# Kernel tuning notes

Measured on AMD Instinct MI355X. Metric: run time of the kernel, lower is better.

The kernel has to match this reference:

```python
import jax, jax.numpy as jnp
import numpy as np

WIN = 8          # window_size
DIM = 96         # embedding dim
HEADS = 3        # num_heads
N = WIN * WIN    # tokens per window
B_ = 8192        # total windows (2 images * 64*64 windows)
NUM_WIN = 4096   # windows per image (mask leading dim)


def _relative_position_index():
    # Same construction as the torch module (meshgrid default 'ij').
    ch = np.arange(WIN)
    coords = np.stack(np.meshgrid(ch, ch, indexing="ij"))          # [2, W, W]
    flat = coords.reshape(2, -1)                                     # [2, N]
    rel = flat[:, :, None] - flat[:, None, :]                        # [2, N, N]
    rel = rel.transpose(1, 2, 0).astype(np.int32)                    # [N, N, 2]
    rel[:, :, 0] += WIN - 1
    rel[:, :, 1] += WIN - 1
    rel[:, :, 0] *= 2 * WIN - 1
    return rel.sum(-1)                                               # [N, N] int32


def setup_inputs() -> dict:
    key = jax.random.key(0)
    ks = jax.random.split(key, 8)
    x = jax.random.normal(ks[0], (B_, N, DIM), dtype=jnp.float32)
    mask = jax.random.normal(ks[1], (NUM_WIN, N, N), dtype=jnp.float32)
    s = 0.02
    qkv_w = jax.random.normal(ks[2], (3 * DIM, DIM), dtype=jnp.float32) * s
    qkv_b = jax.random.normal(ks[3], (3 * DIM,), dtype=jnp.float32) * s
    proj_w = jax.random.normal(ks[4], (DIM, DIM), dtype=jnp.float32) * s
    proj_b = jax.random.normal(ks[5], (DIM,), dtype=jnp.float32) * s
    n_bias = (2 * WIN - 1) * (2 * WIN - 1)  # 225
    bias_table = jax.random.normal(ks[6], (n_bias, HEADS), dtype=jnp.float32) * s
    rel_idx = jnp.asarray(_relative_position_index())  # [N, N] int32
    return {"x": x, "mask": mask, "qkv_w": qkv_w, "qkv_b": qkv_b,
            "proj_w": proj_w, "proj_b": proj_b, "bias_table": bias_table,
            "rel_idx": rel_idx}


def reference(x, mask, qkv_w, qkv_b, proj_w, proj_b, bias_table, rel_idx):
    Bw, n, C = x.shape
    hd = C // HEADS
    scale = hd ** (-0.5)
    qkv = (x @ qkv_w.T + qkv_b).reshape(Bw, n, 3, HEADS, hd)
    qkv = jnp.transpose(qkv, (2, 0, 3, 1, 4))
    q, k, v = qkv[0], qkv[1], qkv[2]
    attn = jnp.einsum("bhqd,bhkd->bhqk", q * scale, k)              # [Bw, H, n, n]
    # relative position bias gather: [n, n, H] -> [H, n, n]
    bias = bias_table[rel_idx.reshape(-1)].reshape(n, n, HEADS)
    attn = attn + jnp.transpose(bias, (2, 0, 1))[None]
    # shift mask: broadcast over (batch, heads)
    nw = mask.shape[0]
    attn = attn.reshape(Bw // nw, nw, HEADS, n, n) + mask[None, :, None]
    attn = attn.reshape(Bw, HEADS, n, n)
    attn = jax.nn.softmax(attn, axis=-1)
    out = jnp.einsum("bhqk,bhkd->bhqd", attn, v)                    # [Bw, H, n, hd]
    out = jnp.transpose(out, (0, 2, 1, 3)).reshape(Bw, n, C)
    return out @ proj_w.T + proj_b
```

## Files before the change

kernel.cpp:

```cpp
#include <hip/hip_runtime.h>

typedef __attribute__((ext_vector_type(8))) short short8v;
typedef __attribute__((ext_vector_type(4))) float f32x4;

#define INVLN2 1.4426950408889634f

__device__ __forceinline__ ushort f2bf(float f) {
  union { float f; unsigned int u; } c; c.f = f;
  return (ushort)((c.u + 0x7FFFu + ((c.u >> 16) & 1u)) >> 16);
}

__device__ __forceinline__ unsigned cvtpk(float a, float b) {
  unsigned r;
  asm("v_cvt_pk_bf16_f32 %0, %1, %2" : "=v"(r) : "v"(a), "v"(b));
  return r;
}

__device__ __forceinline__ float exp2w(float x) {
#if __has_builtin(__builtin_amdgcn_exp2f)
  return __builtin_amdgcn_exp2f(x);
#else
  return __expf(x * 0.6931471805599453f);
#endif
}

__device__ __forceinline__ short8v bits8(unsigned a, unsigned b, unsigned c, unsigned d) {
  union { unsigned u[4]; short8v s; } cv;
  cv.u[0] = a; cv.u[1] = b; cv.u[2] = c; cv.u[3] = d;
  return cv.s;
}

__global__ __launch_bounds__(256) void setup_k(
    const float* __restrict__ qkv_w, const float* __restrict__ proj_w,
    const float* __restrict__ bias_table, const int* __restrict__ rel_idx,
    const float* __restrict__ qkv_b,
    ushort* __restrict__ qkv_wb, ushort* __restrict__ proj_wb,
    float* __restrict__ bias_comb, float* __restrict__ qkv_bs) {
  const float qs = 0.17677669529663687f * INVLN2;
  int idx = blockIdx.x * 256 + threadIdx.x;
  if (idx < 27648) {
    qkv_wb[idx] = f2bf(qkv_w[idx] * (idx < 9216 ? qs : 1.0f));
  } else if (idx < 36864) {
    int i = idx - 27648;
    int cw = i / 96, j = i % 96;
    int h = j >> 5, kk = j & 31;
    int g = kk >> 3, b = (kk & 4) >> 2, d = kk & 3;
    int src = h * 32 + 16 * b + 4 * g + d;
    proj_wb[i] = f2bf(proj_w[cw * 96 + src]);
  } else if (idx < 49152) {
    int i = idx - 36864;
    int h = i / 4096, rc = i % 4096;
    bias_comb[i] = bias_table[rel_idx[rc] * 3 + h] * INVLN2;
  } else if (idx < 49440) {
    int i = idx - 49152;
    qkv_bs[i] = qkv_b[i] * (i < 96 ? qs : 1.0f);
  }
}

__global__ __launch_bounds__(256, 1) void winattn(
    const float* __restrict__ x, const float* __restrict__ mask,
    const ushort* __restrict__ qkv_wb, const ushort* __restrict__ proj_wb,
    const float* __restrict__ bias_comb, const float* __restrict__ qkv_bs,
    const float* __restrict__ proj_b, float* __restrict__ out) {
  __shared__ ushort klds[4][64][104];
  __shared__ ushort vts[4][96][64];
  __shared__ ushort wq[29952];

  const int bb = blockIdx.x;
  const int t = threadIdx.x;
  const int w = t >> 6;
  const int lane = t & 63;
  const int l15 = lane & 15;
  const int g = lane >> 4;
  const int qrow = w * 16 + l15;

  float4 xr4[4][3][2];
  #pragma unroll
  for (int u = 0; u < 4; ++u) {
    const int win = bb + ((u >> 1) << 11) + ((u & 1) << 12);
    const float* xr = x + ((size_t)win * 64 + qrow) * 96 + g * 8;
    #pragma unroll
    for (int ks3 = 0; ks3 < 3; ++ks3) {
      xr4[u][ks3][0] = *reinterpret_cast<const float4*>(xr + ks3 * 32);
      xr4[u][ks3][1] = *reinterpret_cast<const float4*>(xr + ks3 * 32 + 4);
    }
  }
  float4 mk4[2][4];
  #pragma unroll
  for (int p = 0; p < 2; ++p) {
    const float* mrow = mask + (size_t)(bb + (p << 11)) * 4096 + qrow * 64;
    #pragma unroll
    for (int tj = 0; tj < 4; ++tj)
      mk4[p][tj] = *reinterpret_cast<const float4*>(mrow + tj * 16 + g * 4);
  }

  #pragma unroll
  for (int i = 0; i < 14; ++i) {
    const int c = i * 256 + t;
    if (i < 13 || t < 128) {
      const int row = c / 12, cc = c % 12;
      short8v wv = *reinterpret_cast<const short8v*>(qkv_wb + row * 96 + cc * 8);
      *reinterpret_cast<short8v*>(&wq[row * 104 + cc * 8]) = wv;
    }
  }
  __syncthreads();

  short8v xa[4][3];
  #pragma unroll
  for (int u = 0; u < 4; ++u)
    #pragma unroll
    for (int ks3 = 0; ks3 < 3; ++ks3) {
      const float4 a0 = xr4[u][ks3][0], a1 = xr4[u][ks3][1];
      xa[u][ks3] = bits8(cvtpk(a0.x, a0.y), cvtpk(a0.z, a0.w),
                         cvtpk(a1.x, a1.y), cvtpk(a1.z, a1.w));
    }

  unsigned qpk[4][6][2];
  short8v bfA[3];
  float4 qbA = {0.f, 0.f, 0.f, 0.f}, qbB;
  float vbA = 0.f, vbB;
  {
    const ushort* wr = &wq[l15 * 104 + g * 8];
    bfA[0] = *reinterpret_cast<const short8v*>(wr);
    bfA[1] = *reinterpret_cast<const short8v*>(wr + 32);
    bfA[2] = *reinterpret_cast<const short8v*>(wr + 64);
    qbA = *reinterpret_cast<const float4*>(qkv_bs + g * 4);
  }
  #pragma unroll
  for (int nt = 0; nt < 18; ++nt) {
    short8v bfB[3];
    if (nt < 17) {
      const ushort* wr = &wq[((nt + 1) * 16 + l15) * 104 + g * 8];
      bfB[0] = *reinterpret_cast<const short8v*>(wr);
      bfB[1] = *reinterpret_cast<const short8v*>(wr + 32);
      bfB[2] = *reinterpret_cast<const short8v*>(wr + 64);
      if (nt + 1 < 12) qbB = *reinterpret_cast<const float4*>(qkv_bs + (nt + 1) * 16 + g * 4);
      else             vbB = qkv_bs[(nt + 1) * 16 + l15];
    }
    if (nt < 6) {
      #pragma unroll
      for (int u = 0; u < 4; ++u) {
        f32x4 acc = {0.f, 0.f, 0.f, 0.f};
        #pragma unroll
        for (int ks3 = 0; ks3 < 3; ++ks3)
          acc = __builtin_amdgcn_mfma_f32_16x16x32_bf16(bfA[ks3], xa[u][ks3], acc, 0, 0, 0);
        qpk[u][nt][0] = cvtpk(acc[0] + qbA.x, acc[1] + qbA.y);
        qpk[u][nt][1] = cvtpk(acc[2] + qbA.z, acc[3] + qbA.w);
      }
    } else if (nt < 12) {
      const int m = nt - 6;
      const int kcol = 32 * (m >> 1) + 8 * g + 4 * (m & 1);
      #pragma unroll
      for (int u = 0; u < 4; ++u) {
        f32x4 acc = {0.f, 0.f, 0.f, 0.f};
        #pragma unroll
        for (int ks3 = 0; ks3 < 3; ++ks3)
          acc = __builtin_amdgcn_mfma_f32_16x16x32_bf16(bfA[ks3], xa[u][ks3], acc, 0, 0, 0);
        uint2 pk = make_uint2(cvtpk(acc[0] + qbA.x, acc[1] + qbA.y),
                              cvtpk(acc[2] + qbA.z, acc[3] + qbA.w));
        *reinterpret_cast<uint2*>(&klds[u][qrow][kcol]) = pk;
      }
    } else {
      const int vc = nt * 16 + l15 - 192;
      const int tk = (32 * (w >> 1) + 8 * g + 4 * (w & 1)) ^ ((vc & 7) << 3);
      #pragma unroll
      for (int u = 0; u < 4; ++u) {
        f32x4 acc = {0.f, 0.f, 0.f, 0.f};
        #pragma unroll
        for (int ks3 = 0; ks3 < 3; ++ks3)
          acc = __builtin_amdgcn_mfma_f32_16x16x32_bf16(xa[u][ks3], bfA[ks3], acc, 0, 0, 0);
        uint2 pk = make_uint2(cvtpk(acc[0] + vbA, acc[1] + vbA),
                              cvtpk(acc[2] + vbA, acc[3] + vbA));
        *reinterpret_cast<uint2*>(&vts[u][vc][tk]) = pk;
      }
    }
    if (nt < 17) {
      bfA[0] = bfB[0]; bfA[1] = bfB[1]; bfA[2] = bfB[2];
      qbA = qbB; vbA = vbB;
    }
  }

  short8v qf[4][3];
  #pragma unroll
  for (int u = 0; u < 4; ++u)
    #pragma unroll
    for (int h = 0; h < 3; ++h)
      qf[u][h] = bits8(qpk[u][2 * h][0], qpk[u][2 * h][1],
                       qpk[u][2 * h + 1][0], qpk[u][2 * h + 1][1]);

  const float* bcb0 = bias_comb + qrow * 64;
  float bcf[3][4][4];
  #pragma unroll
  for (int h = 0; h < 3; ++h)
    #pragma unroll
    for (int tj = 0; tj < 4; ++tj) {
      float4 b4 = *reinterpret_cast<const float4*>(bcb0 + h * 4096 + tj * 16 + g * 4);
      bcf[h][tj][0] = b4.x; bcf[h][tj][1] = b4.y;
      bcf[h][tj][2] = b4.z; bcf[h][tj][3] = b4.w;
    }
  float mkp[2][4][4];
  #pragma unroll
  for (int p = 0; p < 2; ++p)
    #pragma unroll
    for (int tj = 0; tj < 4; ++tj) {
      mkp[p][tj][0] = mk4[p][tj].x * INVLN2;
      mkp[p][tj][1] = mk4[p][tj].y * INVLN2;
      mkp[p][tj][2] = mk4[p][tj].z * INVLN2;
      mkp[p][tj][3] = mk4[p][tj].w * INVLN2;
    }

  __syncthreads();

  short8v ofv[3][4];

  #pragma unroll
  for (int h = 0; h < 3; ++h) {
    f32x4 s[4][4];
    #pragma unroll
    for (int tj = 0; tj < 4; ++tj) {
      #pragma unroll
      for (int u = 0; u < 4; ++u) {
        short8v kf = *reinterpret_cast<const short8v*>(&klds[u][tj * 16 + l15][h * 32 + g * 8]);
        f32x4 z = {0.f, 0.f, 0.f, 0.f};
        s[u][tj] = __builtin_amdgcn_mfma_f32_16x16x32_bf16(kf, qf[u][h], z, 0, 0, 0);
      }
    }
    #pragma unroll
    for (int tj = 0; tj < 4; ++tj)
      #pragma unroll
      for (int r = 0; r < 4; ++r) {
        const float b0 = bcf[h][tj][r] + mkp[0][tj][r];
        const float b1 = bcf[h][tj][r] + mkp[1][tj][r];
        s[0][tj][r] += b0; s[1][tj][r] += b0;
        s[2][tj][r] += b1; s[3][tj][r] += b1;
      }
    float inv[4];
    #pragma unroll
    for (int u = 0; u < 4; ++u) {
      #pragma unroll
      for (int tj = 0; tj < 4; ++tj)
        #pragma unroll
        for (int r = 0; r < 4; ++r) s[u][tj][r] = exp2w(s[u][tj][r]);
      float sm = ((s[u][0][0] + s[u][0][1]) + (s[u][0][2] + s[u][0][3]))
               + ((s[u][1][0] + s[u][1][1]) + (s[u][1][2] + s[u][1][3]))
               + ((s[u][2][0] + s[u][2][1]) + (s[u][2][2] + s[u][2][3]))
               + ((s[u][3][0] + s[u][3][1]) + (s[u][3][2] + s[u][3][3]));
      sm += __shfl_xor(sm, 16);
      sm += __shfl_xor(sm, 32);
      inv[u] = __builtin_amdgcn_rcpf(sm);
    }
    short8v pfv[4][2];
    #pragma unroll
    for (int u = 0; u < 4; ++u) {
      unsigned p00 = cvtpk(s[u][0][0], s[u][0][1]);
      unsigned p01 = cvtpk(s[u][0][2], s[u][0][3]);
      unsigned p10 = cvtpk(s[u][1][0], s[u][1][1]);
      unsigned p11 = cvtpk(s[u][1][2], s[u][1][3]);
      unsigned p20 = cvtpk(s[u][2][0], s[u][2][1]);
      unsigned p21 = cvtpk(s[u][2][2], s[u][2][3]);
      unsigned p30 = cvtpk(s[u][3][0], s[u][3][1]);
      unsigned p31 = cvtpk(s[u][3][2], s[u][3][3]);
      pfv[u][0] = bits8(p00, p01, p10, p11);
      pfv[u][1] = bits8(p20, p21, p30, p31);
    }
    #pragma unroll
    for (int u = 0; u < 4; ++u) {
      f32x4 oacc[2];
      #pragma unroll
      for (int nt = 0; nt < 2; ++nt) {
        const int vc = h * 32 + nt * 16 + l15;
        f32x4 o = {0.f, 0.f, 0.f, 0.f};
        #pragma unroll
        for (int ks2 = 0; ks2 < 2; ++ks2) {
          const int tk = (ks2 * 32 + g * 8) ^ ((vc & 7) << 3);
          short8v vf = *reinterpret_cast<const short8v*>(&vts[u][vc][tk]);
          o = __builtin_amdgcn_mfma_f32_16x16x32_bf16(vf, pfv[u][ks2], o, 0, 0, 0);
        }
        oacc[nt] = o;
      }
      unsigned o00 = cvtpk(oacc[0][0] * inv[u], oacc[0][1] * inv[u]);
      unsigned o01 = cvtpk(oacc[0][2] * inv[u], oacc[0][3] * inv[u]);
      unsigned o10 = cvtpk(oacc[1][0] * inv[u], oacc[1][1] * inv[u]);
      unsigned o11 = cvtpk(oacc[1][2] * inv[u], oacc[1][3] * inv[u]);
      ofv[h][u] = bits8(o00, o01, o10, o11);
    }
  }

  f32x4 pacc[4][6];
  #pragma unroll
  for (int u = 0; u < 4; ++u)
    #pragma unroll
    for (int nt2 = 0; nt2 < 6; ++nt2) pacc[u][nt2] = (f32x4){0.f, 0.f, 0.f, 0.f};
  #pragma unroll
  for (int h = 0; h < 3; ++h) {
    #pragma unroll
    for (int nt2 = 0; nt2 < 6; ++nt2) {
      short8v pfw = *reinterpret_cast<const short8v*>(proj_wb + (nt2 * 16 + l15) * 96 + h * 32 + g * 8);
      #pragma unroll
      for (int u = 0; u < 4; ++u)
        pacc[u][nt2] = __builtin_amdgcn_mfma_f32_16x16x32_bf16(ofv[h][u], pfw, pacc[u][nt2], 0, 0, 0);
    }
  }

  float pb[6];
  #pragma unroll
  for (int nt2 = 0; nt2 < 6; ++nt2) pb[nt2] = proj_b[nt2 * 16 + l15];
  #pragma unroll
  for (int u = 0; u < 4; ++u) {
    const int win = bb + ((u >> 1) << 11) + ((u & 1) << 12);
    float* ob = out + (size_t)win * 6144 + (w * 16 + g * 4) * 96 + l15;
    #pragma unroll
    for (int nt2 = 0; nt2 < 6; ++nt2)
      #pragma unroll
      for (int r = 0; r < 4; ++r)
        ob[r * 96 + nt2 * 16] = pacc[u][nt2][r] + pb[nt2];
  }
}

extern "C" void kernel_launch(void* const* d_in, const int* in_sizes, int n_in,
                              void* d_out, int out_size, void* d_ws, size_t ws_size,
                              hipStream_t stream) {
  const float* x          = (const float*)d_in[0];
  const float* mask       = (const float*)d_in[1];
  const float* qkv_w      = (const float*)d_in[2];
  const float* qkv_b      = (const float*)d_in[3];
  const float* proj_w     = (const float*)d_in[4];
  const float* proj_b     = (const float*)d_in[5];
  const float* bias_table = (const float*)d_in[6];
  const int*   rel_idx    = (const int*)d_in[7];

  char* ws = (char*)d_ws;
  ushort* qkv_wb    = (ushort*)ws;
  ushort* proj_wb   = (ushort*)(ws + 55296);
  float*  bias_comb = (float*)(ws + 55296 + 18432);
  float*  qkv_bs    = (float*)(ws + 55296 + 18432 + 49152);

  setup_k<<<194, 256, 0, stream>>>(qkv_w, proj_w, bias_table, rel_idx, qkv_b,
                                   qkv_wb, proj_wb, bias_comb, qkv_bs);
  winattn<<<2048, 256, 0, stream>>>(x, mask, qkv_wb, proj_wb,
                                    bias_comb, qkv_bs, proj_b, (float*)d_out);
}
```

Baseline: 160.2 us.

## Make blocks process four window groups with register prefetch of next inputs

Each block now loops over four consecutive window groups instead of one, launching a quarter as many blocks. The bf16 QKV weights are staged into shared memory once per block and reused. The x and mask loads for the next group are issued right after the QKV stage so they overlap attention and projection compute. Extra barriers guard reuse of the K/V shared buffers, and holding the prefetched data in registers adds register pressure and coarser load balancing.

```diff
diff --git a/kernel.cpp b/kernel.cpp
--- a/kernel.cpp
+++ b/kernel.cpp
@@ -66,7 +66,6 @@
   __shared__ ushort vts[4][96][64];
   __shared__ ushort wq[29952];
 
-  const int bb = blockIdx.x;
   const int t = threadIdx.x;
   const int w = t >> 6;
   const int lane = t & 63;
@@ -75,23 +74,26 @@
   const int qrow = w * 16 + l15;
 
   float4 xr4[4][3][2];
-  #pragma unroll
-  for (int u = 0; u < 4; ++u) {
-    const int win = bb + ((u >> 1) << 11) + ((u & 1) << 12);
-    const float* xr = x + ((size_t)win * 64 + qrow) * 96 + g * 8;
-    #pragma unroll
-    for (int ks3 = 0; ks3 < 3; ++ks3) {
-      xr4[u][ks3][0] = *reinterpret_cast<const float4*>(xr + ks3 * 32);
-      xr4[u][ks3][1] = *reinterpret_cast<const float4*>(xr + ks3 * 32 + 4);
-    }
-  }
   float4 mk4[2][4];
-  #pragma unroll
-  for (int p = 0; p < 2; ++p) {
-    const float* mrow = mask + (size_t)(bb + (p << 11)) * 4096 + qrow * 64;
-    #pragma unroll
-    for (int tj = 0; tj < 4; ++tj)
-      mk4[p][tj] = *reinterpret_cast<const float4*>(mrow + tj * 16 + g * 4);
+  {
+    const int bb0 = blockIdx.x * 4;
+    #pragma unroll
+    for (int u = 0; u < 4; ++u) {
+      const int win = bb0 + ((u >> 1) << 11) + ((u & 1) << 12);
+      const float* xr = x + ((size_t)win * 64 + qrow) * 96 + g * 8;
+      #pragma unroll
+      for (int ks3 = 0; ks3 < 3; ++ks3) {
+        xr4[u][ks3][0] = *reinterpret_cast<const float4*>(xr + ks3 * 32);
+        xr4[u][ks3][1] = *reinterpret_cast<const float4*>(xr + ks3 * 32 + 4);
+      }
+    }
+    #pragma unroll
+    for (int p = 0; p < 2; ++p) {
+      const float* mrow = mask + (size_t)(bb0 + (p << 11)) * 4096 + qrow * 64;
+      #pragma unroll
+      for (int tj = 0; tj < 4; ++tj)
+        mk4[p][tj] = *reinterpret_cast<const float4*>(mrow + tj * 16 + g * 4);
+    }
   }
 
   #pragma unroll
@@ -105,89 +107,6 @@
   }
   __syncthreads();
 
-  short8v xa[4][3];
-  #pragma unroll
-  for (int u = 0; u < 4; ++u)
-    #pragma unroll
-    for (int ks3 = 0; ks3 < 3; ++ks3) {
-      const float4 a0 = xr4[u][ks3][0], a1 = xr4[u][ks3][1];
-      xa[u][ks3] = bits8(cvtpk(a0.x, a0.y), cvtpk(a0.z, a0.w),
-                         cvtpk(a1.x, a1.y), cvtpk(a1.z, a1.w));
-    }
-
-  unsigned qpk[4][6][2];
-  short8v bfA[3];
-  float4 qbA = {0.f, 0.f, 0.f, 0.f}, qbB;
-  float vbA = 0.f, vbB;
-  {
-    const ushort* wr = &wq[l15 * 104 + g * 8];
-    bfA[0] = *reinterpret_cast<const short8v*>(wr);
-    bfA[1] = *reinterpret_cast<const short8v*>(wr + 32);
-    bfA[2] = *reinterpret_cast<const short8v*>(wr + 64);
-    qbA = *reinterpret_cast<const float4*>(qkv_bs + g * 4);
-  }
-  #pragma unroll
-  for (int nt = 0; nt < 18; ++nt) {
-    short8v bfB[3];
-    if (nt < 17) {
-      const ushort* wr = &wq[((nt + 1) * 16 + l15) * 104 + g * 8];
-      bfB[0] = *reinterpret_cast<const short8v*>(wr);
-      bfB[1] = *reinterpret_cast<const short8v*>(wr + 32);
-      bfB[2] = *reinterpret_cast<const short8v*>(wr + 64);
-      if (nt + 1 < 12) qbB = *reinterpret_cast<const float4*>(qkv_bs + (nt + 1) * 16 + g * 4);
-      else             vbB = qkv_bs[(nt + 1) * 16 + l15];
-    }
-    if (nt < 6) {
-      #pragma unroll
-      for (int u = 0; u < 4; ++u) {
-        f32x4 acc = {0.f, 0.f, 0.f, 0.f};
-        #pragma unroll
-        for (int ks3 = 0; ks3 < 3; ++ks3)
-          acc = __builtin_amdgcn_mfma_f32_16x16x32_bf16(bfA[ks3], xa[u][ks3], acc, 0, 0, 0);
-        qpk[u][nt][0] = cvtpk(acc[0] + qbA.x, acc[1] + qbA.y);
-        qpk[u][nt][1] = cvtpk(acc[2] + qbA.z, acc[3] + qbA.w);
-      }
-    } else if (nt < 12) {
-      const int m = nt - 6;
-      const int kcol = 32 * (m >> 1) + 8 * g + 4 * (m & 1);
-      #pragma unroll
-      for (int u = 0; u < 4; ++u) {
-        f32x4 acc = {0.f, 0.f, 0.f, 0.f};
-        #pragma unroll
-        for (int ks3 = 0; ks3 < 3; ++ks3)
-          acc = __builtin_amdgcn_mfma_f32_16x16x32_bf16(bfA[ks3], xa[u][ks3], acc, 0, 0, 0);
-        uint2 pk = make_uint2(cvtpk(acc[0] + qbA.x, acc[1] + qbA.y),
-                              cvtpk(acc[2] + qbA.z, acc[3] + qbA.w));
-        *reinterpret_cast<uint2*>(&klds[u][qrow][kcol]) = pk;
-      }
-    } else {
-      const int vc = nt * 16 + l15 - 192;
-      const int tk = (32 * (w >> 1) + 8 * g + 4 * (w & 1)) ^ ((vc & 7) << 3);
-      #pragma unroll
-      for (int u = 0; u < 4; ++u) {
-        f32x4 acc = {0.f, 0.f, 0.f, 0.f};
-        #pragma unroll
-        for (int ks3 = 0; ks3 < 3; ++ks3)
-          acc = __builtin_amdgcn_mfma_f32_16x16x32_bf16(xa[u][ks3], bfA[ks3], acc, 0, 0, 0);
-        uint2 pk = make_uint2(cvtpk(acc[0] + vbA, acc[1] + vbA),
-                              cvtpk(acc[2] + vbA, acc[3] + vbA));
-        *reinterpret_cast<uint2*>(&vts[u][vc][tk]) = pk;
-      }
-    }
-    if (nt < 17) {
-      bfA[0] = bfB[0]; bfA[1] = bfB[1]; bfA[2] = bfB[2];
-      qbA = qbB; vbA = vbB;
-    }
-  }
-
-  short8v qf[4][3];
-  #pragma unroll
-  for (int u = 0; u < 4; ++u)
-    #pragma unroll
-    for (int h = 0; h < 3; ++h)
-      qf[u][h] = bits8(qpk[u][2 * h][0], qpk[u][2 * h][1],
-                       qpk[u][2 * h + 1][0], qpk[u][2 * h + 1][1]);
-
   const float* bcb0 = bias_comb + qrow * 64;
   float bcf[3][4][4];
   #pragma unroll
@@ -198,122 +117,232 @@
       bcf[h][tj][0] = b4.x; bcf[h][tj][1] = b4.y;
       bcf[h][tj][2] = b4.z; bcf[h][tj][3] = b4.w;
     }
-  float mkp[2][4][4];
-  #pragma unroll
-  for (int p = 0; p < 2; ++p)
-    #pragma unroll
-    for (int tj = 0; tj < 4; ++tj) {
-      mkp[p][tj][0] = mk4[p][tj].x * INVLN2;
-      mkp[p][tj][1] = mk4[p][tj].y * INVLN2;
-      mkp[p][tj][2] = mk4[p][tj].z * INVLN2;
-      mkp[p][tj][3] = mk4[p][tj].w * INVLN2;
-    }
-
-  __syncthreads();
-
-  short8v ofv[3][4];
-
-  #pragma unroll
-  for (int h = 0; h < 3; ++h) {
-    f32x4 s[4][4];
-    #pragma unroll
-    for (int tj = 0; tj < 4; ++tj) {
-      #pragma unroll
-      for (int u = 0; u < 4; ++u) {
-        short8v kf = *reinterpret_cast<const short8v*>(&klds[u][tj * 16 + l15][h * 32 + g * 8]);
-        f32x4 z = {0.f, 0.f, 0.f, 0.f};
-        s[u][tj] = __builtin_amdgcn_mfma_f32_16x16x32_bf16(kf, qf[u][h], z, 0, 0, 0);
-      }
-    }
-    #pragma unroll
-    for (int tj = 0; tj < 4; ++tj)
-      #pragma unroll
-      for (int r = 0; r < 4; ++r) {
-        const float b0 = bcf[h][tj][r] + mkp[0][tj][r];
-        const float b1 = bcf[h][tj][r] + mkp[1][tj][r];
-        s[0][tj][r] += b0; s[1][tj][r] += b0;
-        s[2][tj][r] += b1; s[3][tj][r] += b1;
-      }
-    float inv[4];
-    #pragma unroll
-    for (int u = 0; u < 4; ++u) {
-      #pragma unroll
-      for (int tj = 0; tj < 4; ++tj)
-        #pragma unroll
-        for (int r = 0; r < 4; ++r) s[u][tj][r] = exp2w(s[u][tj][r]);
-      float sm = ((s[u][0][0] + s[u][0][1]) + (s[u][0][2] + s[u][0][3]))
-               + ((s[u][1][0] + s[u][1][1]) + (s[u][1][2] + s[u][1][3]))
-               + ((s[u][2][0] + s[u][2][1]) + (s[u][2][2] + s[u][2][3]))
-               + ((s[u][3][0] + s[u][3][1]) + (s[u][3][2] + s[u][3][3]));
-      sm += __shfl_xor(sm, 16);
-      sm += __shfl_xor(sm, 32);
-      inv[u] = __builtin_amdgcn_rcpf(sm);
-    }
-    short8v pfv[4][2];
-    #pragma unroll
-    for (int u = 0; u < 4; ++u) {
-      unsigned p00 = cvtpk(s[u][0][0], s[u][0][1]);
-      unsigned p01 = cvtpk(s[u][0][2], s[u][0][3]);
-      unsigned p10 = cvtpk(s[u][1][0], s[u][1][1]);
-      unsigned p11 = cvtpk(s[u][1][2], s[u][1][3]);
-      unsigned p20 = cvtpk(s[u][2][0], s[u][2][1]);
-      unsigned p21 = cvtpk(s[u][2][2], s[u][2][3]);
-      unsigned p30 = cvtpk(s[u][3][0], s[u][3][1]);
-      unsigned p31 = cvtpk(s[u][3][2], s[u][3][3]);
-      pfv[u][0] = bits8(p00, p01, p10, p11);
-      pfv[u][1] = bits8(p20, p21, p30, p31);
-    }
-    #pragma unroll
-    for (int u = 0; u < 4; ++u) {
-      f32x4 oacc[2];
-      #pragma unroll
-      for (int nt = 0; nt < 2; ++nt) {
-        const int vc = h * 32 + nt * 16 + l15;
-        f32x4 o = {0.f, 0.f, 0.f, 0.f};
-        #pragma unroll
-        for (int ks2 = 0; ks2 < 2; ++ks2) {
-          const int tk = (ks2 * 32 + g * 8) ^ ((vc & 7) << 3);
-          short8v vf = *reinterpret_cast<const short8v*>(&vts[u][vc][tk]);
-          o = __builtin_amdgcn_mfma_f32_16x16x32_bf16(vf, pfv[u][ks2], o, 0, 0, 0);
-        }
-        oacc[nt] = o;
-      }
-      unsigned o00 = cvtpk(oacc[0][0] * inv[u], oacc[0][1] * inv[u]);
-      unsigned o01 = cvtpk(oacc[0][2] * inv[u], oacc[0][3] * inv[u]);
-      unsigned o10 = cvtpk(oacc[1][0] * inv[u], oacc[1][1] * inv[u]);
-      unsigned o11 = cvtpk(oacc[1][2] * inv[u], oacc[1][3] * inv[u]);
-      ofv[h][u] = bits8(o00, o01, o10, o11);
-    }
-  }
-
-  f32x4 pacc[4][6];
-  #pragma unroll
-  for (int u = 0; u < 4; ++u)
-    #pragma unroll
-    for (int nt2 = 0; nt2 < 6; ++nt2) pacc[u][nt2] = (f32x4){0.f, 0.f, 0.f, 0.f};
-  #pragma unroll
-  for (int h = 0; h < 3; ++h) {
-    #pragma unroll
-    for (int nt2 = 0; nt2 < 6; ++nt2) {
-      short8v pfw = *reinterpret_cast<const short8v*>(proj_wb + (nt2 * 16 + l15) * 96 + h * 32 + g * 8);
-      #pragma unroll
-      for (int u = 0; u < 4; ++u)
-        pacc[u][nt2] = __builtin_amdgcn_mfma_f32_16x16x32_bf16(ofv[h][u], pfw, pacc[u][nt2], 0, 0, 0);
-    }
-  }
-
   float pb[6];
   #pragma unroll
   for (int nt2 = 0; nt2 < 6; ++nt2) pb[nt2] = proj_b[nt2 * 16 + l15];
-  #pragma unroll
-  for (int u = 0; u < 4; ++u) {
-    const int win = bb + ((u >> 1) << 11) + ((u & 1) << 12);
-    float* ob = out + (size_t)win * 6144 + (w * 16 + g * 4) * 96 + l15;
-    #pragma unroll
-    for (int nt2 = 0; nt2 < 6; ++nt2)
-      #pragma unroll
-      for (int r = 0; r < 4; ++r)
-        ob[r * 96 + nt2 * 16] = pacc[u][nt2][r] + pb[nt2];
+
+  for (int j = 0; j < 4; ++j) {
+    const int bb = blockIdx.x * 4 + j;
+
+    short8v xa[4][3];
+    #pragma unroll
+    for (int u = 0; u < 4; ++u)
+      #pragma unroll
+      for (int ks3 = 0; ks3 < 3; ++ks3) {
+        const float4 a0 = xr4[u][ks3][0], a1 = xr4[u][ks3][1];
+        xa[u][ks3] = bits8(cvtpk(a0.x, a0.y), cvtpk(a0.z, a0.w),
+                           cvtpk(a1.x, a1.y), cvtpk(a1.z, a1.w));
+      }
+    float mkp[2][4][4];
+    #pragma unroll
+    for (int p = 0; p < 2; ++p)
+      #pragma unroll
+      for (int tj = 0; tj < 4; ++tj) {
+        mkp[p][tj][0] = mk4[p][tj].x * INVLN2;
+        mkp[p][tj][1] = mk4[p][tj].y * INVLN2;
+        mkp[p][tj][2] = mk4[p][tj].z * INVLN2;
+        mkp[p][tj][3] = mk4[p][tj].w * INVLN2;
+      }
+
+    unsigned qpk[4][6][2];
+    short8v bfA[3];
+    float4 qbA = {0.f, 0.f, 0.f, 0.f}, qbB;
+    float vbA = 0.f, vbB;
+    {
+      const ushort* wr = &wq[l15 * 104 + g * 8];
+      bfA[0] = *reinterpret_cast<const short8v*>(wr);
+      bfA[1] = *reinterpret_cast<const short8v*>(wr + 32);
+      bfA[2] = *reinterpret_cast<const short8v*>(wr + 64);
+      qbA = *reinterpret_cast<const float4*>(qkv_bs + g * 4);
+    }
+    #pragma unroll
+    for (int nt = 0; nt < 18; ++nt) {
+      short8v bfB[3];
+      if (nt < 17) {
+        const ushort* wr = &wq[((nt + 1) * 16 + l15) * 104 + g * 8];
+        bfB[0] = *reinterpret_cast<const short8v*>(wr);
+        bfB[1] = *reinterpret_cast<const short8v*>(wr + 32);
+        bfB[2] = *reinterpret_cast<const short8v*>(wr + 64);
+        if (nt + 1 < 12) qbB = *reinterpret_cast<const float4*>(qkv_bs + (nt + 1) * 16 + g * 4);
+        else             vbB = qkv_bs[(nt + 1) * 16 + l15];
+      }
+      if (nt < 6) {
+        #pragma unroll
+        for (int u = 0; u < 4; ++u) {
+          f32x4 acc = {0.f, 0.f, 0.f, 0.f};
+          #pragma unroll
+          for (int ks3 = 0; ks3 < 3; ++ks3)
+            acc = __builtin_amdgcn_mfma_f32_16x16x32_bf16(bfA[ks3], xa[u][ks3], acc, 0, 0, 0);
+          qpk[u][nt][0] = cvtpk(acc[0] + qbA.x, acc[1] + qbA.y);
+          qpk[u][nt][1] = cvtpk(acc[2] + qbA.z, acc[3] + qbA.w);
+        }
+      } else if (nt < 12) {
+        const int m = nt - 6;
+        const int kcol = 32 * (m >> 1) + 8 * g + 4 * (m & 1);
+        #pragma unroll
+        for (int u = 0; u < 4; ++u) {
+          f32x4 acc = {0.f, 0.f, 0.f, 0.f};
+          #pragma unroll
+          for (int ks3 = 0; ks3 < 3; ++ks3)
+            acc = __builtin_amdgcn_mfma_f32_16x16x32_bf16(bfA[ks3], xa[u][ks3], acc, 0, 0, 0);
+          uint2 pk = make_uint2(cvtpk(acc[0] + qbA.x, acc[1] + qbA.y),
+                                cvtpk(acc[2] + qbA.z, acc[3] + qbA.w));
+          *reinterpret_cast<uint2*>(&klds[u][qrow][kcol]) = pk;
+        }
+      } else {
+        const int vc = nt * 16 + l15 - 192;
+        const int tk = (32 * (w >> 1) + 8 * g + 4 * (w & 1)) ^ ((vc & 7) << 3);
+        #pragma unroll
+        for (int u = 0; u < 4; ++u) {
+          f32x4 acc = {0.f, 0.f, 0.f, 0.f};
+          #pragma unroll
+          for (int ks3 = 0; ks3 < 3; ++ks3)
+            acc = __builtin_amdgcn_mfma_f32_16x16x32_bf16(xa[u][ks3], bfA[ks3], acc, 0, 0, 0);
+          uint2 pk = make_uint2(cvtpk(acc[0] + vbA, acc[1] + vbA),
+                                cvtpk(acc[2] + vbA, acc[3] + vbA));
+          *reinterpret_cast<uint2*>(&vts[u][vc][tk]) = pk;
+        }
+      }
+      if (nt < 17) {
+        bfA[0] = bfB[0]; bfA[1] = bfB[1]; bfA[2] = bfB[2];
+        qbA = qbB; vbA = vbB;
+      }
+    }
+
+    short8v qf[4][3];
+    #pragma unroll
+    for (int u = 0; u < 4; ++u)
+      #pragma unroll
+      for (int h = 0; h < 3; ++h)
+        qf[u][h] = bits8(qpk[u][2 * h][0], qpk[u][2 * h][1],
+                         qpk[u][2 * h + 1][0], qpk[u][2 * h + 1][1]);
+
+    __syncthreads();
+
+    if (j < 3) {
+      const int bbn = bb + 1;
+      #pragma unroll
+      for (int u = 0; u < 4; ++u) {
+        const int win = bbn + ((u >> 1) << 11) + ((u & 1) << 12);
+        const float* xr = x + ((size_t)win * 64 + qrow) * 96 + g * 8;
+        #pragma unroll
+        for (int ks3 = 0; ks3 < 3; ++ks3) {
+          xr4[u][ks3][0] = *reinterpret_cast<const float4*>(xr + ks3 * 32);
+          xr4[u][ks3][1] = *reinterpret_cast<const float4*>(xr + ks3 * 32 + 4);
+        }
+      }
+      #pragma unroll
+      for (int p = 0; p < 2; ++p) {
+        const float* mrow = mask + (size_t)(bbn + (p << 11)) * 4096 + qrow * 64;
+        #pragma unroll
+        for (int tj = 0; tj < 4; ++tj)
+          mk4[p][tj] = *reinterpret_cast<const float4*>(mrow + tj * 16 + g * 4);
+      }
+    }
+
+    short8v ofv[3][4];
+
+    #pragma unroll
+    for (int h = 0; h < 3; ++h) {
+      f32x4 s[4][4];
+      #pragma unroll
+      for (int tj = 0; tj < 4; ++tj) {
+        #pragma unroll
+        for (int u = 0; u < 4; ++u) {
+          short8v kf = *reinterpret_cast<const short8v*>(&klds[u][tj * 16 + l15][h * 32 + g * 8]);
+          f32x4 z = {0.f, 0.f, 0.f, 0.f};
+          s[u][tj] = __builtin_amdgcn_mfma_f32_16x16x32_bf16(kf, qf[u][h], z, 0, 0, 0);
+        }
+      }
+      #pragma unroll
+      for (int tj = 0; tj < 4; ++tj)
+        #pragma unroll
+        for (int r = 0; r < 4; ++r) {
+          const float b0 = bcf[h][tj][r] + mkp[0][tj][r];
+          const float b1 = bcf[h][tj][r] + mkp[1][tj][r];
+          s[0][tj][r] += b0; s[1][tj][r] += b0;
+          s[2][tj][r] += b1; s[3][tj][r] += b1;
+        }
+      float inv[4];
+      #pragma unroll
+      for (int u = 0; u < 4; ++u) {
+        #pragma unroll
+        for (int tj = 0; tj < 4; ++tj)
+          #pragma unroll
+          for (int r = 0; r < 4; ++r) s[u][tj][r] = exp2w(s[u][tj][r]);
+        float sm = ((s[u][0][0] + s[u][0][1]) + (s[u][0][2] + s[u][0][3]))
+                 + ((s[u][1][0] + s[u][1][1]) + (s[u][1][2] + s[u][1][3]))
+                 + ((s[u][2][0] + s[u][2][1]) + (s[u][2][2] + s[u][2][3]))
+                 + ((s[u][3][0] + s[u][3][1]) + (s[u][3][2] + s[u][3][3]));
+        sm += __shfl_xor(sm, 16);
+        sm += __shfl_xor(sm, 32);
+        inv[u] = __builtin_amdgcn_rcpf(sm);
+      }
+      short8v pfv[4][2];
+      #pragma unroll
+      for (int u = 0; u < 4; ++u) {
+        unsigned p00 = cvtpk(s[u][0][0], s[u][0][1]);
+        unsigned p01 = cvtpk(s[u][0][2], s[u][0][3]);
+        unsigned p10 = cvtpk(s[u][1][0], s[u][1][1]);
+        unsigned p11 = cvtpk(s[u][1][2], s[u][1][3]);
+        unsigned p20 = cvtpk(s[u][2][0], s[u][2][1]);
+        unsigned p21 = cvtpk(s[u][2][2], s[u][2][3]);
+        unsigned p30 = cvtpk(s[u][3][0], s[u][3][1]);
+        unsigned p31 = cvtpk(s[u][3][2], s[u][3][3]);
+        pfv[u][0] = bits8(p00, p01, p10, p11);
+        pfv[u][1] = bits8(p20, p21, p30, p31);
+      }
+      #pragma unroll
+      for (int u = 0; u < 4; ++u) {
+        f32x4 oacc[2];
+        #pragma unroll
+        for (int nt = 0; nt < 2; ++nt) {
+          const int vc = h * 32 + nt * 16 + l15;
+          f32x4 o = {0.f, 0.f, 0.f, 0.f};
+          #pragma unroll
+          for (int ks2 = 0; ks2 < 2; ++ks2) {
+            const int tk = (ks2 * 32 + g * 8) ^ ((vc & 7) << 3);
+            short8v vf = *reinterpret_cast<const short8v*>(&vts[u][vc][tk]);
+            o = __builtin_amdgcn_mfma_f32_16x16x32_bf16(vf, pfv[u][ks2], o, 0, 0, 0);
+          }
+          oacc[nt] = o;
+        }
+        unsigned o00 = cvtpk(oacc[0][0] * inv[u], oacc[0][1] * inv[u]);
+        unsigned o01 = cvtpk(oacc[0][2] * inv[u], oacc[0][3] * inv[u]);
+        unsigned o10 = cvtpk(oacc[1][0] * inv[u], oacc[1][1] * inv[u]);
+        unsigned o11 = cvtpk(oacc[1][2] * inv[u], oacc[1][3] * inv[u]);
+        ofv[h][u] = bits8(o00, o01, o10, o11);
+      }
+    }
+
+    f32x4 pacc[4][6];
+    #pragma unroll
+    for (int u = 0; u < 4; ++u)
+      #pragma unroll
+      for (int nt2 = 0; nt2 < 6; ++nt2) pacc[u][nt2] = (f32x4){0.f, 0.f, 0.f, 0.f};
+    #pragma unroll
+    for (int h = 0; h < 3; ++h) {
+      #pragma unroll
+      for (int nt2 = 0; nt2 < 6; ++nt2) {
+        short8v pfw = *reinterpret_cast<const short8v*>(proj_wb + (nt2 * 16 + l15) * 96 + h * 32 + g * 8);
+        #pragma unroll
+        for (int u = 0; u < 4; ++u)
+          pacc[u][nt2] = __builtin_amdgcn_mfma_f32_16x16x32_bf16(ofv[h][u], pfw, pacc[u][nt2], 0, 0, 0);
+      }
+    }
+
+    __syncthreads();
+
+    #pragma unroll
+    for (int u = 0; u < 4; ++u) {
+      const int win = bb + ((u >> 1) << 11) + ((u & 1) << 12);
+      float* ob = out + (size_t)win * 6144 + (w * 16 + g * 4) * 96 + l15;
+      #pragma unroll
+      for (int nt2 = 0; nt2 < 6; ++nt2)
+        #pragma unroll
+        for (int r = 0; r < 4; ++r)
+          ob[r * 96 + nt2 * 16] = pacc[u][nt2][r] + pb[nt2];
+    }
   }
 }
 
@@ -337,6 +366,6 @@
 
   setup_k<<<194, 256, 0, stream>>>(qkv_w, proj_w, bias_table, rel_idx, qkv_b,
                                    qkv_wb, proj_wb, bias_comb, qkv_bs);
-  winattn<<<2048, 256, 0, stream>>>(x, mask, qkv_wb, proj_wb,
-                                    bias_comb, qkv_bs, proj_b, (float*)d_out);
-}
+  winattn<<<512, 256, 0, stream>>>(x, mask, qkv_wb, proj_wb,
+                                   bias_comb, qkv_bs, proj_b, (float*)d_out);
+}
```

Result: slower. 173.4 us (+8.2%).
